# Optimization experiments

Hardware: AMD Instinct MI355X
Metric: run time of the kernel (lower is better)

## Reference

```python
import jax, jax.numpy as jnp
import numpy as np

NUM_HEADS = 16
HEAD_DIM = 64
Q_DIM = K_DIM = V_DIM = 1024
LQ = LK = 4096
TAU = HEAD_DIM ** (-0.5)


def setup_inputs() -> dict:
    key = jax.random.key(0)
    ks = jax.random.split(key, 11)
    inner = NUM_HEADS * HEAD_DIM
    s = 0.02
    return {
        "q": jax.random.normal(ks[0], (LQ, Q_DIM), dtype=jnp.float32),
        "k": jax.random.normal(ks[1], (LK, K_DIM), dtype=jnp.float32),
        "v": jax.random.normal(ks[2], (LK, V_DIM), dtype=jnp.float32),
        "Wq": jax.random.normal(ks[3], (Q_DIM, inner), dtype=jnp.float32) * s,
        "bq": jax.random.normal(ks[4], (inner,), dtype=jnp.float32) * s,
        "Wk": jax.random.normal(ks[5], (K_DIM, inner), dtype=jnp.float32) * s,
        "bk": jax.random.normal(ks[6], (inner,), dtype=jnp.float32) * s,
        "Wv": jax.random.normal(ks[7], (V_DIM, inner), dtype=jnp.float32) * s,
        "bv": jax.random.normal(ks[8], (inner,), dtype=jnp.float32) * s,
        "Wo": jax.random.normal(ks[9], (inner, Q_DIM), dtype=jnp.float32) * s,
        "bo": jax.random.normal(ks[10], (Q_DIM,), dtype=jnp.float32) * s,
    }


def reference(q, k, v, Wq, bq, Wk, bk, Wv, bv, Wo, bo):
    h, x = NUM_HEADS, HEAD_DIM
    # projections: [L, h*x] -> per-head layout
    qh = (q @ Wq + bq).reshape(-1, h, x)  # [Lq, h, x]
    kh = (k @ Wk + bk).reshape(-1, h, x)  # [Lk, h, x]
    vh = (v @ Wv + bv).reshape(-1, h, x)  # [Lk, h, x]
    # scores: [h, Lq, Lk]
    att = jnp.einsum('qhx,khx->hqk', qh, kh) * TAU
    att = jax.nn.softmax(att, axis=-1)  # dropout=0.0 -> identity
    ctx = jnp.einsum('hqk,khx->qhx', att, vh).reshape(-1, h * x)  # [Lq, h*x]
    out = ctx @ Wo + bo  # [Lq, Q_DIM]
    return out, att
```

## Files before the change

kernel.cpp:

```cpp
#include <hip/hip_runtime.h>
#include <hip/hip_bf16.h>

typedef unsigned short ushort_t;
typedef __attribute__((ext_vector_type(8))) short short8;
typedef __attribute__((ext_vector_type(8))) __bf16 bf16x8;
typedef __attribute__((ext_vector_type(4))) float f32x4;

#define LQS 4096
#define LKS 4096
#define NH 16
#define HD 64
#define DIN 1024
static constexpr float TAU_S = 0.125f;

__device__ __forceinline__ ushort_t f32_to_bf16(float x) {
  union { float f; unsigned u; } v; v.f = x;
  unsigned r = v.u + 0x7FFF + ((v.u >> 16) & 1);
  return (ushort_t)(r >> 16);
}

__device__ __forceinline__ void gld_lds16(const void* g, void* l) {
  __builtin_amdgcn_global_load_lds((const __attribute__((address_space(1))) void*)g,
                                   (__attribute__((address_space(3))) void*)l, 16, 0, 0);
}

__device__ __forceinline__ f32x4 mfma16(bf16x8 a, bf16x8 b, f32x4 c) {
  return __builtin_amdgcn_mfma_f32_16x16x32_bf16(a, b, c, 0, 0, 0);
}

__global__ void cvt_kernel(const float* __restrict__ src, ushort_t* __restrict__ dst, int n) {
  int i = (blockIdx.x * 256 + threadIdx.x) * 8;
  if (i + 8 > n) return;
  float4 a = *(const float4*)(src + i);
  float4 b = *(const float4*)(src + i + 4);
  short8 o;
  o[0] = (short)f32_to_bf16(a.x); o[1] = (short)f32_to_bf16(a.y);
  o[2] = (short)f32_to_bf16(a.z); o[3] = (short)f32_to_bf16(a.w);
  o[4] = (short)f32_to_bf16(b.x); o[5] = (short)f32_to_bf16(b.y);
  o[6] = (short)f32_to_bf16(b.z); o[7] = (short)f32_to_bf16(b.w);
  *(short8*)(dst + i) = o;
}

__global__ void transpose_w(const float* __restrict__ W, ushort_t* __restrict__ Wt) {
  __shared__ float tile[64][65];
  const int t = threadIdx.x;
  const int k0 = blockIdx.y * 64, n0 = blockIdx.x * 64;
#pragma unroll
  for (int i = 0; i < 16; ++i) {
    int idx = i * 256 + t;
    int r = idx >> 6, c = idx & 63;
    tile[r][c] = W[(size_t)(k0 + r) * DIN + n0 + c];
  }
  __syncthreads();
#pragma unroll
  for (int i = 0; i < 16; ++i) {
    int idx = i * 256 + t;
    int r = idx >> 6, c = idx & 63;
    Wt[(size_t)(n0 + r) * DIN + k0 + c] = f32_to_bf16(tile[c][r]);
  }
}

__global__ void transpose_v(const ushort_t* __restrict__ vh, ushort_t* __restrict__ vt) {
  __shared__ ushort_t tile[64][65];
  const int t = threadIdx.x;
  const int k0 = blockIdx.x * 64, h = blockIdx.y;
#pragma unroll
  for (int i = 0; i < 16; ++i) {
    int idx = i * 256 + t;
    int r = idx >> 6, c = idx & 63;
    tile[r][c] = vh[(size_t)(k0 + r) * DIN + h * HD + c];
  }
  __syncthreads();
#pragma unroll
  for (int i = 0; i < 16; ++i) {
    int idx = i * 256 + t;
    int r = idx >> 6, c = idx & 63;
    vt[((size_t)h * HD + r) * (size_t)LKS + k0 + c] = tile[c][r];
  }
}

template <bool OUT_F32>
__launch_bounds__(256, 2)
__global__ void gemm_nt(const ushort_t* __restrict__ A, const ushort_t* __restrict__ Bt,
                        const float* __restrict__ bias, void* __restrict__ Cout,
                        int M, int N, int K, float scale) {
  __shared__ __align__(16) ushort_t Alds[128 * 64];
  __shared__ __align__(16) ushort_t Blds[128 * 64];
  const int t = threadIdx.x, wave = t >> 6, lane = t & 63;
  const int l15 = lane & 15, lg = lane >> 4;
  const int m0 = blockIdx.y * 128, n0 = blockIdx.x * 128;
  const int wr = wave >> 1, wc = wave & 1;
  f32x4 acc[4][4];
#pragma unroll
  for (int i = 0; i < 4; ++i)
#pragma unroll
    for (int j = 0; j < 4; ++j) acc[i][j] = (f32x4){0.f, 0.f, 0.f, 0.f};

  for (int tk = 0; tk < K / 64; ++tk) {
#pragma unroll
    for (int c = 0; c < 4; ++c) {
      int chunk = wave * 4 + c;
      int row = chunk * 8 + (lane >> 3);
      int ss = (lane & 7) ^ (row & 7);
      gld_lds16(A + (size_t)(m0 + row) * K + tk * 64 + ss * 8, (char*)Alds + chunk * 1024);
      gld_lds16(Bt + (size_t)(n0 + row) * K + tk * 64 + ss * 8, (char*)Blds + chunk * 1024);
    }
    __syncthreads();
#pragma unroll
    for (int kk = 0; kk < 2; ++kk) {
      bf16x8 a[4], b[4];
#pragma unroll
      for (int i = 0; i < 4; ++i) {
        int ra = wr * 64 + i * 16 + l15;
        a[i] = *(const bf16x8*)((const char*)Alds + ra * 128 + ((((kk * 4 + lg) << 4)) ^ ((ra & 7) << 4)));
        int rb = wc * 64 + i * 16 + l15;
        b[i] = *(const bf16x8*)((const char*)Blds + rb * 128 + ((((kk * 4 + lg) << 4)) ^ ((rb & 7) << 4)));
      }
#pragma unroll
      for (int mi = 0; mi < 4; ++mi)
#pragma unroll
        for (int ni = 0; ni < 4; ++ni)
          acc[mi][ni] = mfma16(a[mi], b[ni], acc[mi][ni]);
    }
    __syncthreads();
  }
#pragma unroll
  for (int ni = 0; ni < 4; ++ni) {
    int coln = n0 + wc * 64 + ni * 16 + l15;
    float bv = bias[coln];
#pragma unroll
    for (int mi = 0; mi < 4; ++mi) {
#pragma unroll
      for (int r = 0; r < 4; ++r) {
        int rowm = m0 + wr * 64 + mi * 16 + lg * 4 + r;
        float v = (acc[mi][ni][r] + bv) * scale;
        if (OUT_F32)
          ((float*)Cout)[(size_t)rowm * N + coln] = v;
        else
          ((ushort_t*)Cout)[(size_t)rowm * N + coln] = f32_to_bf16(v);
      }
    }
  }
}

__launch_bounds__(256, 2)
__global__ void attn_kernel(const ushort_t* __restrict__ qh, const ushort_t* __restrict__ kh,
                            const ushort_t* __restrict__ vt, float* __restrict__ att,
                            ushort_t* __restrict__ ctx) {
  __shared__ __align__(16) ushort_t Klds[64 * 64];
  __shared__ __align__(16) ushort_t Vlds[64 * 64];
  __shared__ __align__(16) ushort_t Plds[64 * 64];
  const int t = threadIdx.x, wave = t >> 6, lane = t & 63;
  const int l15 = lane & 15, lg = lane >> 4;
  const int h = blockIdx.y;
  const int q0 = blockIdx.x * 64;

  bf16x8 qa[2];
  {
    int row = q0 + wave * 16 + l15;
    const ushort_t* qp = qh + (size_t)row * DIN + h * HD + lg * 8;
    qa[0] = *(const bf16x8*)(qp);
    qa[1] = *(const bf16x8*)(qp + 32);
  }

  float rs[4] = {0.f, 0.f, 0.f, 0.f};
  for (int tk = 0; tk < LKS / 64; ++tk) {
#pragma unroll
    for (int c = 0; c < 2; ++c) {
      int chunk = wave * 2 + c;
      int row = chunk * 8 + (lane >> 3);
      int ss = (lane & 7) ^ (row & 7);
      gld_lds16(kh + (size_t)(tk * 64 + row) * DIN + h * HD + ss * 8, (char*)Klds + chunk * 1024);
    }
    __syncthreads();
#pragma unroll
    for (int ct = 0; ct < 4; ++ct) {
      f32x4 acc = (f32x4){0.f, 0.f, 0.f, 0.f};
#pragma unroll
      for (int kk = 0; kk < 2; ++kk) {
        int row = ct * 16 + l15;
        bf16x8 kb = *(const bf16x8*)((const char*)Klds + row * 128 + ((((kk * 4 + lg) << 4)) ^ ((row & 7) << 4)));
        acc = mfma16(qa[kk], kb, acc);
      }
#pragma unroll
      for (int r = 0; r < 4; ++r) rs[r] += __expf(acc[r]);
    }
    __syncthreads();
  }
#pragma unroll
  for (int m = 1; m < 16; m <<= 1) {
#pragma unroll
    for (int r = 0; r < 4; ++r) rs[r] += __shfl_xor(rs[r], m, 64);
  }
  float recip[4];
#pragma unroll
  for (int r = 0; r < 4; ++r) recip[r] = 1.0f / rs[r];

  f32x4 cacc[4];
#pragma unroll
  for (int x = 0; x < 4; ++x) cacc[x] = (f32x4){0.f, 0.f, 0.f, 0.f};
  float* atth = att + ((size_t)h << 24);

  for (int tk = 0; tk < LKS / 64; ++tk) {
#pragma unroll
    for (int c = 0; c < 2; ++c) {
      int chunk = wave * 2 + c;
      int row = chunk * 8 + (lane >> 3);
      int ss = (lane & 7) ^ (row & 7);
      gld_lds16(kh + (size_t)(tk * 64 + row) * DIN + h * HD + ss * 8, (char*)Klds + chunk * 1024);
      gld_lds16(vt + ((size_t)h * HD + row) * (size_t)LKS + tk * 64 + ss * 8, (char*)Vlds + chunk * 1024);
    }
    __syncthreads();
#pragma unroll
    for (int ct = 0; ct < 4; ++ct) {
      f32x4 acc = (f32x4){0.f, 0.f, 0.f, 0.f};
#pragma unroll
      for (int kk = 0; kk < 2; ++kk) {
        int row = ct * 16 + l15;
        bf16x8 kb = *(const bf16x8*)((const char*)Klds + row * 128 + ((((kk * 4 + lg) << 4)) ^ ((row & 7) << 4)));
        acc = mfma16(qa[kk], kb, acc);
      }
#pragma unroll
      for (int r = 0; r < 4; ++r) {
        float p = __expf(acc[r]) * recip[r];
        int rowq = q0 + wave * 16 + lg * 4 + r;
        int col = tk * 64 + ct * 16 + l15;
        atth[((size_t)rowq << 12) + col] = p;
        int R = wave * 16 + lg * 4 + r;
        int byte = R * 128 + ((ct * 32 + l15 * 2) ^ ((R & 7) << 4));
        *(ushort_t*)((char*)Plds + byte) = f32_to_bf16(p);
      }
    }
    bf16x8 pa[2];
#pragma unroll
    for (int kk = 0; kk < 2; ++kk) {
      int R = wave * 16 + l15;
      pa[kk] = *(const bf16x8*)((const char*)Plds + R * 128 + ((((kk * 4 + lg) << 4)) ^ ((R & 7) << 4)));
    }
#pragma unroll
    for (int x = 0; x < 4; ++x) {
#pragma unroll
      for (int kk = 0; kk < 2; ++kk) {
        int rv = x * 16 + l15;
        bf16x8 vb = *(const bf16x8*)((const char*)Vlds + rv * 128 + ((((kk * 4 + lg) << 4)) ^ ((rv & 7) << 4)));
        cacc[x] = mfma16(pa[kk], vb, cacc[x]);
      }
    }
    __syncthreads();
  }
#pragma unroll
  for (int x = 0; x < 4; ++x) {
#pragma unroll
    for (int r = 0; r < 4; ++r) {
      int rowq = q0 + wave * 16 + lg * 4 + r;
      int col = h * HD + x * 16 + l15;
      ctx[(size_t)rowq * DIN + col] = f32_to_bf16(cacc[x][r]);
    }
  }
}

extern "C" void kernel_launch(void* const* d_in, const int* in_sizes, int n_in,
                              void* d_out, int out_size, void* d_ws, size_t ws_size,
                              hipStream_t stream) {
  const float* q = (const float*)d_in[0];
  const float* k = (const float*)d_in[1];
  const float* v = (const float*)d_in[2];
  const float* Wq = (const float*)d_in[3];
  const float* bq = (const float*)d_in[4];
  const float* Wk = (const float*)d_in[5];
  const float* bk = (const float*)d_in[6];
  const float* Wv = (const float*)d_in[7];
  const float* bv = (const float*)d_in[8];
  const float* Wo = (const float*)d_in[9];
  const float* bo = (const float*)d_in[10];

  float* out = (float*)d_out;
  float* att = out + (size_t)LQS * DIN;

  char* ws = (char*)d_ws;
  ushort_t* qhb = (ushort_t*)(ws + (size_t)0);
  ushort_t* khb = (ushort_t*)(ws + ((size_t)8 << 20));
  ushort_t* vhb = (ushort_t*)(ws + ((size_t)16 << 20));
  ushort_t* vtb = (ushort_t*)(ws + ((size_t)24 << 20));
  ushort_t* ctx = (ushort_t*)(ws + ((size_t)32 << 20));
  ushort_t* qb = (ushort_t*)(ws + ((size_t)40 << 20));
  ushort_t* kb = (ushort_t*)(ws + ((size_t)48 << 20));
  ushort_t* vb = (ushort_t*)(ws + ((size_t)56 << 20));
  ushort_t* Wqt = (ushort_t*)(ws + ((size_t)64 << 20));
  ushort_t* Wkt = (ushort_t*)(ws + ((size_t)66 << 20));
  ushort_t* Wvt = (ushort_t*)(ws + ((size_t)68 << 20));
  ushort_t* Wot = (ushort_t*)(ws + ((size_t)70 << 20));

  const int n = LQS * DIN;
  cvt_kernel<<<n / 8 / 256, 256, 0, stream>>>(q, qb, n);
  cvt_kernel<<<n / 8 / 256, 256, 0, stream>>>(k, kb, n);
  cvt_kernel<<<n / 8 / 256, 256, 0, stream>>>(v, vb, n);

  dim3 tg(16, 16);
  transpose_w<<<tg, 256, 0, stream>>>(Wq, Wqt);
  transpose_w<<<tg, 256, 0, stream>>>(Wk, Wkt);
  transpose_w<<<tg, 256, 0, stream>>>(Wv, Wvt);
  transpose_w<<<tg, 256, 0, stream>>>(Wo, Wot);

  dim3 gg(DIN / 128, LQS / 128);
  gemm_nt<false><<<gg, 256, 0, stream>>>(qb, Wqt, bq, qhb, LQS, DIN, DIN, TAU_S);
  gemm_nt<false><<<gg, 256, 0, stream>>>(kb, Wkt, bk, khb, LQS, DIN, DIN, 1.0f);
  gemm_nt<false><<<gg, 256, 0, stream>>>(vb, Wvt, bv, vhb, LQS, DIN, DIN, 1.0f);

  transpose_v<<<dim3(64, 16), 256, 0, stream>>>(vhb, vtb);

  attn_kernel<<<dim3(LQS / 64, NH), 256, 0, stream>>>(qhb, khb, vtb, att, ctx);

  gemm_nt<true><<<gg, 256, 0, stream>>>(ctx, Wot, bo, out, LQS, DIN, DIN, 1.0f);
}
```

Baseline: 472.6 us.

## Enlarge attention tiles to 128x128 and fold log2e into exp2 softmax

The attention kernel now uses 512-thread blocks covering 128 queries, and walks K/V in 128-key tiles with a matching V/P LDS layout and swizzle. Each K/V load is reused across twice as many queries. The Q projection scale now folds in log2(e), so softmax uses the hardware exp2 instruction instead of __expf. Projection GEMMs switch to 128x64 tiles to launch more blocks. MFMA sections are wrapped in s_setprio, and the fp32 attention-matrix and output stores become nontemporal to reduce cache pollution from the large write stream. Larger LDS and the higher thread count may limit occupancy.

```diff
diff --git a/kernel.cpp b/kernel.cpp
--- a/kernel.cpp
+++ b/kernel.cpp
@@ -11,7 +11,12 @@
 #define NH 16
 #define HD 64
 #define DIN 1024
+#define QBLK 128
+#define KVBLK 128
 static constexpr float TAU_S = 0.125f;
+static constexpr float LOG2E = 1.4426950408889634f;
+
+__device__ __forceinline__ float exp2_fast(float x) { return __builtin_amdgcn_exp2f(x); }
 
 __device__ __forceinline__ ushort_t f32_to_bf16(float x) {
   union { float f; unsigned u; } v; v.f = x;
@@ -85,16 +90,16 @@
                         const float* __restrict__ bias, void* __restrict__ Cout,
                         int M, int N, int K, float scale) {
   __shared__ __align__(16) ushort_t Alds[128 * 64];
-  __shared__ __align__(16) ushort_t Blds[128 * 64];
+  __shared__ __align__(16) ushort_t Blds[64 * 64];
   const int t = threadIdx.x, wave = t >> 6, lane = t & 63;
   const int l15 = lane & 15, lg = lane >> 4;
-  const int m0 = blockIdx.y * 128, n0 = blockIdx.x * 128;
+  const int m0 = blockIdx.y * 128, n0 = blockIdx.x * 64;
   const int wr = wave >> 1, wc = wave & 1;
-  f32x4 acc[4][4];
+  f32x4 acc[4][2];
 #pragma unroll
   for (int i = 0; i < 4; ++i)
 #pragma unroll
-    for (int j = 0; j < 4; ++j) acc[i][j] = (f32x4){0.f, 0.f, 0.f, 0.f};
+    for (int j = 0; j < 2; ++j) acc[i][j] = (f32x4){0.f, 0.f, 0.f, 0.f};
 
   for (int tk = 0; tk < K / 64; ++tk) {
 #pragma unroll
@@ -103,30 +108,41 @@
       int row = chunk * 8 + (lane >> 3);
       int ss = (lane & 7) ^ (row & 7);
       gld_lds16(A + (size_t)(m0 + row) * K + tk * 64 + ss * 8, (char*)Alds + chunk * 1024);
+    }
+#pragma unroll
+    for (int c = 0; c < 2; ++c) {
+      int chunk = wave * 2 + c;
+      int row = chunk * 8 + (lane >> 3);
+      int ss = (lane & 7) ^ (row & 7);
       gld_lds16(Bt + (size_t)(n0 + row) * K + tk * 64 + ss * 8, (char*)Blds + chunk * 1024);
     }
     __syncthreads();
+    bf16x8 a[4], b[2];
 #pragma unroll
     for (int kk = 0; kk < 2; ++kk) {
-      bf16x8 a[4], b[4];
 #pragma unroll
       for (int i = 0; i < 4; ++i) {
         int ra = wr * 64 + i * 16 + l15;
         a[i] = *(const bf16x8*)((const char*)Alds + ra * 128 + ((((kk * 4 + lg) << 4)) ^ ((ra & 7) << 4)));
-        int rb = wc * 64 + i * 16 + l15;
-        b[i] = *(const bf16x8*)((const char*)Blds + rb * 128 + ((((kk * 4 + lg) << 4)) ^ ((rb & 7) << 4)));
-      }
+      }
+#pragma unroll
+      for (int j = 0; j < 2; ++j) {
+        int rb = wc * 32 + j * 16 + l15;
+        b[j] = *(const bf16x8*)((const char*)Blds + rb * 128 + ((((kk * 4 + lg) << 4)) ^ ((rb & 7) << 4)));
+      }
+      __builtin_amdgcn_s_setprio(1);
 #pragma unroll
       for (int mi = 0; mi < 4; ++mi)
 #pragma unroll
-        for (int ni = 0; ni < 4; ++ni)
+        for (int ni = 0; ni < 2; ++ni)
           acc[mi][ni] = mfma16(a[mi], b[ni], acc[mi][ni]);
-    }
-    __syncthreads();
-  }
-#pragma unroll
-  for (int ni = 0; ni < 4; ++ni) {
-    int coln = n0 + wc * 64 + ni * 16 + l15;
+      __builtin_amdgcn_s_setprio(0);
+    }
+    __syncthreads();
+  }
+#pragma unroll
+  for (int ni = 0; ni < 2; ++ni) {
+    int coln = n0 + wc * 32 + ni * 16 + l15;
     float bv = bias[coln];
 #pragma unroll
     for (int mi = 0; mi < 4; ++mi) {
@@ -135,7 +151,7 @@
         int rowm = m0 + wr * 64 + mi * 16 + lg * 4 + r;
         float v = (acc[mi][ni][r] + bv) * scale;
         if (OUT_F32)
-          ((float*)Cout)[(size_t)rowm * N + coln] = v;
+          __builtin_nontemporal_store(v, (float*)Cout + (size_t)rowm * N + coln);
         else
           ((ushort_t*)Cout)[(size_t)rowm * N + coln] = f32_to_bf16(v);
       }
@@ -143,17 +159,17 @@
   }
 }
 
-__launch_bounds__(256, 2)
+__launch_bounds__(512, 4)
 __global__ void attn_kernel(const ushort_t* __restrict__ qh, const ushort_t* __restrict__ kh,
                             const ushort_t* __restrict__ vt, float* __restrict__ att,
                             ushort_t* __restrict__ ctx) {
-  __shared__ __align__(16) ushort_t Klds[64 * 64];
-  __shared__ __align__(16) ushort_t Vlds[64 * 64];
-  __shared__ __align__(16) ushort_t Plds[64 * 64];
+  __shared__ __align__(16) ushort_t Klds[KVBLK * 64];
+  __shared__ __align__(16) ushort_t Vlds[64 * KVBLK];
+  __shared__ __align__(16) ushort_t Plds[QBLK * KVBLK];
   const int t = threadIdx.x, wave = t >> 6, lane = t & 63;
   const int l15 = lane & 15, lg = lane >> 4;
   const int h = blockIdx.y;
-  const int q0 = blockIdx.x * 64;
+  const int q0 = blockIdx.x * QBLK;
 
   bf16x8 qa[2];
   {
@@ -164,26 +180,28 @@
   }
 
   float rs[4] = {0.f, 0.f, 0.f, 0.f};
-  for (int tk = 0; tk < LKS / 64; ++tk) {
+  for (int tk = 0; tk < LKS / KVBLK; ++tk) {
 #pragma unroll
     for (int c = 0; c < 2; ++c) {
       int chunk = wave * 2 + c;
       int row = chunk * 8 + (lane >> 3);
       int ss = (lane & 7) ^ (row & 7);
-      gld_lds16(kh + (size_t)(tk * 64 + row) * DIN + h * HD + ss * 8, (char*)Klds + chunk * 1024);
-    }
-    __syncthreads();
-#pragma unroll
-    for (int ct = 0; ct < 4; ++ct) {
+      gld_lds16(kh + (size_t)(tk * KVBLK + row) * DIN + h * HD + ss * 8, (char*)Klds + chunk * 1024);
+    }
+    __syncthreads();
+#pragma unroll
+    for (int ct = 0; ct < 8; ++ct) {
       f32x4 acc = (f32x4){0.f, 0.f, 0.f, 0.f};
+      __builtin_amdgcn_s_setprio(1);
 #pragma unroll
       for (int kk = 0; kk < 2; ++kk) {
         int row = ct * 16 + l15;
         bf16x8 kb = *(const bf16x8*)((const char*)Klds + row * 128 + ((((kk * 4 + lg) << 4)) ^ ((row & 7) << 4)));
         acc = mfma16(qa[kk], kb, acc);
       }
-#pragma unroll
-      for (int r = 0; r < 4; ++r) rs[r] += __expf(acc[r]);
+      __builtin_amdgcn_s_setprio(0);
+#pragma unroll
+      for (int r = 0; r < 4; ++r) rs[r] += exp2_fast(acc[r]);
     }
     __syncthreads();
   }
@@ -201,51 +219,61 @@
   for (int x = 0; x < 4; ++x) cacc[x] = (f32x4){0.f, 0.f, 0.f, 0.f};
   float* atth = att + ((size_t)h << 24);
 
-  for (int tk = 0; tk < LKS / 64; ++tk) {
+  for (int tk = 0; tk < LKS / KVBLK; ++tk) {
 #pragma unroll
     for (int c = 0; c < 2; ++c) {
       int chunk = wave * 2 + c;
       int row = chunk * 8 + (lane >> 3);
       int ss = (lane & 7) ^ (row & 7);
-      gld_lds16(kh + (size_t)(tk * 64 + row) * DIN + h * HD + ss * 8, (char*)Klds + chunk * 1024);
-      gld_lds16(vt + ((size_t)h * HD + row) * (size_t)LKS + tk * 64 + ss * 8, (char*)Vlds + chunk * 1024);
-    }
-    __syncthreads();
-#pragma unroll
-    for (int ct = 0; ct < 4; ++ct) {
+      gld_lds16(kh + (size_t)(tk * KVBLK + row) * DIN + h * HD + ss * 8, (char*)Klds + chunk * 1024);
+    }
+#pragma unroll
+    for (int c = 0; c < 2; ++c) {
+      int chunk = wave * 2 + c;
+      int xr = chunk * 4 + (lane >> 4);
+      int ks = ((lane & 15) ^ (xr & 7)) * 8;
+      gld_lds16(vt + ((size_t)h * HD + xr) * (size_t)LKS + tk * KVBLK + ks, (char*)Vlds + chunk * 1024);
+    }
+    __syncthreads();
+#pragma unroll
+    for (int ct = 0; ct < 8; ++ct) {
       f32x4 acc = (f32x4){0.f, 0.f, 0.f, 0.f};
+      __builtin_amdgcn_s_setprio(1);
 #pragma unroll
       for (int kk = 0; kk < 2; ++kk) {
         int row = ct * 16 + l15;
         bf16x8 kb = *(const bf16x8*)((const char*)Klds + row * 128 + ((((kk * 4 + lg) << 4)) ^ ((row & 7) << 4)));
         acc = mfma16(qa[kk], kb, acc);
       }
+      __builtin_amdgcn_s_setprio(0);
 #pragma unroll
       for (int r = 0; r < 4; ++r) {
-        float p = __expf(acc[r]) * recip[r];
+        float p = exp2_fast(acc[r]) * recip[r];
         int rowq = q0 + wave * 16 + lg * 4 + r;
-        int col = tk * 64 + ct * 16 + l15;
-        atth[((size_t)rowq << 12) + col] = p;
+        int col = tk * KVBLK + ct * 16 + l15;
+        __builtin_nontemporal_store(p, atth + ((size_t)rowq << 12) + col);
         int R = wave * 16 + lg * 4 + r;
-        int byte = R * 128 + ((ct * 32 + l15 * 2) ^ ((R & 7) << 4));
+        int byte = R * 256 + ((ct * 32 + l15 * 2) ^ ((R & 7) << 4));
         *(ushort_t*)((char*)Plds + byte) = f32_to_bf16(p);
       }
     }
-    bf16x8 pa[2];
-#pragma unroll
-    for (int kk = 0; kk < 2; ++kk) {
+    bf16x8 pa[4];
+#pragma unroll
+    for (int kk = 0; kk < 4; ++kk) {
       int R = wave * 16 + l15;
-      pa[kk] = *(const bf16x8*)((const char*)Plds + R * 128 + ((((kk * 4 + lg) << 4)) ^ ((R & 7) << 4)));
-    }
+      pa[kk] = *(const bf16x8*)((const char*)Plds + R * 256 + (((kk * 64 + lg * 16)) ^ ((R & 7) << 4)));
+    }
+    __builtin_amdgcn_s_setprio(1);
 #pragma unroll
     for (int x = 0; x < 4; ++x) {
 #pragma unroll
-      for (int kk = 0; kk < 2; ++kk) {
+      for (int kk = 0; kk < 4; ++kk) {
         int rv = x * 16 + l15;
-        bf16x8 vb = *(const bf16x8*)((const char*)Vlds + rv * 128 + ((((kk * 4 + lg) << 4)) ^ ((rv & 7) << 4)));
+        bf16x8 vb = *(const bf16x8*)((const char*)Vlds + rv * 256 + (((kk * 64 + lg * 16)) ^ ((rv & 7) << 4)));
         cacc[x] = mfma16(pa[kk], vb, cacc[x]);
       }
     }
+    __builtin_amdgcn_s_setprio(0);
     __syncthreads();
   }
 #pragma unroll
@@ -302,14 +330,14 @@
   transpose_w<<<tg, 256, 0, stream>>>(Wv, Wvt);
   transpose_w<<<tg, 256, 0, stream>>>(Wo, Wot);
 
-  dim3 gg(DIN / 128, LQS / 128);
-  gemm_nt<false><<<gg, 256, 0, stream>>>(qb, Wqt, bq, qhb, LQS, DIN, DIN, TAU_S);
+  dim3 gg(DIN / 64, LQS / 128);
+  gemm_nt<false><<<gg, 256, 0, stream>>>(qb, Wqt, bq, qhb, LQS, DIN, DIN, TAU_S * LOG2E);
   gemm_nt<false><<<gg, 256, 0, stream>>>(kb, Wkt, bk, khb, LQS, DIN, DIN, 1.0f);
   gemm_nt<false><<<gg, 256, 0, stream>>>(vb, Wvt, bv, vhb, LQS, DIN, DIN, 1.0f);
 
   transpose_v<<<dim3(64, 16), 256, 0, stream>>>(vhb, vtb);
 
-  attn_kernel<<<dim3(LQS / 64, NH), 256, 0, stream>>>(qhb, khb, vtb, att, ctx);
+  attn_kernel<<<dim3(LQS / QBLK, NH), 512, 0, stream>>>(qhb, khb, vtb, att, ctx);
 
   gemm_nt<true><<<gg, 256, 0, stream>>>(ctx, Wot, bo, out, LQS, DIN, DIN, 1.0f);
 }
```

Result: slower. 650.5 us (+37.6%).
